# Kernel optimization log

Measured on AMD Instinct MI355X. Metric: run time of the kernel, lower is better.

## Reference

```python
import jax, jax.numpy as jnp
import numpy as np


def setup_inputs() -> dict:
    key = jax.random.key(0)
    k1, k2, k3, k4, k5 = jax.random.split(key, 5)
    B, K, S, E, I, D = 4, 2, 512, 8, 1024, 2048
    x = jax.random.normal(k1, (B, S, I), dtype=jnp.float32)
    weights = jax.random.uniform(k2, (B, K, S), dtype=jnp.float32)
    ensembles = jax.random.randint(k3, (B, K, S), 0, E, dtype=jnp.int64)
    # xavier_uniform-style init for expert weight tables
    lim1 = float(np.sqrt(6.0 / (D + I)))
    proj_in = jax.random.uniform(k4, (E, D, I), dtype=jnp.float32, minval=-lim1, maxval=lim1)
    proj_out = jax.random.uniform(k5, (E, I, D), dtype=jnp.float32, minval=-lim1, maxval=lim1)
    return {"x": x, "weights": weights, "ensembles": ensembles,
            "proj_in": proj_in, "proj_out": proj_out}


def reference(x, weights, ensembles, proj_in, proj_out):
    # x: (B,S,I); weights/ensembles: (B,K,S); proj_in: (E,D,I); proj_out: (E,I,D)
    # Same math as the torch module (dropout = identity in eval):
    #   per token t, out = sum_k w[k,t] * W2[e_kt] @ relu(W1[e_kt] @ x[t])
    # Computed as all-expert batched GEMMs + a gated (one-hot scatter) combine,
    # which is mathematically identical and avoids the (B,K,S,D,I) gather blowup.
    E = proj_in.shape[0]
    h = jax.nn.relu(jnp.einsum('edi,bsi->bsed', proj_in, x))      # (B,S,E,D)
    o = jnp.einsum('eid,bsed->bsei', proj_out, h)                 # (B,S,E,I)
    onehot = jax.nn.one_hot(ensembles, E, dtype=x.dtype)          # (B,K,S,E)
    gate = jnp.einsum('bks,bkse->bse', weights, onehot)           # (B,S,E)
    return jnp.einsum('bsei,bse->bsi', o, gate)                   # (B,S,I)
```

## Files before the change

kernel.cpp:

```cpp
#include <hip/hip_runtime.h>
#include <stdint.h>

#define THREADS 512
#define NE 8
#define BB 4
#define SS 512
#define KK 2
#define II 1024
#define DD 2048
#define NTOK (BB * SS)
#define NASSIGN (BB * KK * SS)

#define F4_X (NTOK * II / 4)
#define F4_P (NE * DD * II / 4)
#define CVB_X (F4_X / 1024)
#define CVB_P (F4_P / 1024)
#define CVB_TOTAL (CVB_X + 2 * CVB_P)

typedef unsigned short u16;
typedef __attribute__((ext_vector_type(8))) __bf16 bf16x8;
typedef __attribute__((ext_vector_type(4))) float f32x4;
typedef __attribute__((ext_vector_type(4))) unsigned int u32x4;

__device__ __forceinline__ u16 f32_to_bf16(float f) {
    unsigned int u = __builtin_bit_cast(unsigned int, f);
    unsigned int r = u + 0x7FFFu + ((u >> 16) & 1u);
    return (u16)(r >> 16);
}

__device__ __forceinline__ unsigned int pk2(float a, float b) {
    return (unsigned int)f32_to_bf16(a) | ((unsigned int)f32_to_bf16(b) << 16);
}

__device__ __forceinline__ void gload16(const void* g, void* l) {
    __builtin_amdgcn_global_load_lds(
        (const __attribute__((address_space(1))) unsigned int*)g,
        (__attribute__((address_space(3))) unsigned int*)l, 16, 0, 0);
}

#define BARRIER() do { \
    __builtin_amdgcn_sched_barrier(0); \
    __builtin_amdgcn_s_barrier(); \
    __builtin_amdgcn_sched_barrier(0); } while (0)

__device__ void setup_body(const void* __restrict__ ens_raw,
                           const float* __restrict__ weights,
                           int* __restrict__ meta,
                           int* __restrict__ tok,
                           float* __restrict__ wgt) {
    __shared__ int s_cnt[NE];
    __shared__ int s_cur[NE];
    __shared__ int s_flag;
    const int t = threadIdx.x;
    if (t < NE) s_cnt[t] = 0;
    if (t == 0) s_flag = 0;
    __syncthreads();

    const unsigned int* w32 = (const unsigned int*)ens_raw;
    unsigned int f = 0;
    for (int i = t; i < NASSIGN / 2; i += 256) f |= w32[2 * i + 1];
    if (f) atomicOr(&s_flag, 1);
    __syncthreads();
    const bool is32 = (s_flag != 0);
    const int* e32 = (const int*)ens_raw;
    const long long* e64 = (const long long*)ens_raw;

    for (int a = t; a < NASSIGN; a += 256) {
        int e = is32 ? e32[a] : (int)e64[a];
        atomicAdd(&s_cnt[e & 7], 1);
    }
    __syncthreads();

    if (t == 0) {
        int pb = 0, nt = 0;
        for (int e = 0; e < NE; e++) {
            int c = s_cnt[e];
            meta[8 + e] = c;
            meta[16 + e] = pb;
            s_cur[e] = pb;
            int n128 = (c + 127) >> 7;
            int pe = pb + n128 * 128;
            for (int i2 = 0; i2 < n128; i2 += 2) {
                meta[32 + nt] = e;
                meta[64 + nt] = pb + i2 * 128;
                meta[96 + nt] = pb + c;
                meta[128 + nt] = pe;
                nt++;
            }
            pb = pe;
        }
        meta[0] = nt;
        meta[1] = pb;
    }
    __syncthreads();

    for (int a = t; a < NASSIGN; a += 256) {
        int e = is32 ? e32[a] : (int)e64[a];
        e &= 7;
        int slot = atomicAdd(&s_cur[e], 1);
        int b = a >> 10;
        int s = a & (SS - 1);
        tok[slot] = b * SS + s;
        wgt[slot] = weights[a];
    }
    __syncthreads();

    for (int e = 0; e < NE; e++) {
        int st = meta[16 + e] + meta[8 + e];
        int en = (e < NE - 1) ? meta[16 + e + 1] : meta[1];
        for (int i = st + t; i < en; i += 256) {
            tok[i] = 0;
            wgt[i] = 0.f;
        }
    }
}

__global__ __launch_bounds__(256)
void convert_setup(const float* __restrict__ x,
                   const float* __restrict__ pin,
                   const float* __restrict__ pout,
                   u16* __restrict__ xb,
                   u16* __restrict__ pb1,
                   u16* __restrict__ pb2,
                   const void* __restrict__ ens,
                   const float* __restrict__ weights,
                   int* __restrict__ meta,
                   int* __restrict__ tok,
                   float* __restrict__ wgt) {
    const int b = blockIdx.x;
    if (b >= CVB_TOTAL) {
        setup_body(ens, weights, meta, tok, wgt);
        return;
    }
    const float* s;
    u16* d;
    size_t base;
    if (b < CVB_X)             { s = x;    d = xb;  base = (size_t)b * 1024; }
    else if (b < CVB_X + CVB_P){ s = pin;  d = pb1; base = (size_t)(b - CVB_X) * 1024; }
    else                       { s = pout; d = pb2; base = (size_t)(b - CVB_X - CVB_P) * 1024; }
    const f32x4* s4 = (const f32x4*)s;
    f32x4 v[4];
#pragma unroll
    for (int q = 0; q < 4; q++)
        v[q] = __builtin_nontemporal_load(&s4[base + q * 256 + threadIdx.x]);
#pragma unroll
    for (int q = 0; q < 4; q++) {
        uint2 o;
        o.x = pk2(v[q][0], v[q][1]);
        o.y = pk2(v[q][2], v[q][3]);
        *(uint2*)(d + 4 * (base + q * 256 + threadIdx.x)) = o;
    }
}

__global__ __launch_bounds__(THREADS, 2)
void gemm1(const u16* __restrict__ Abase,
           const u16* __restrict__ Bbase,
           const int* __restrict__ meta,
           const int* __restrict__ tok,
           u16* __restrict__ hdst) {
    constexpr int NT = II / 64;
    constexpr int ASZ = 256 * 64 * 2;
    constexpr int BUFSZ = 2 * ASZ;
    __shared__ char smem[2 * BUFSZ];

    const int lid = blockIdx.x;
    const int g = lid & 7;
    const int i = lid >> 3;
    const int tile = g + 8 * (i % 3);
    const int colt = i / 3;
    if (tile >= meta[0]) return;

    const int e     = meta[32 + tile];
    const int sbase = meta[64 + tile];
    const int wend  = meta[128 + tile];
    const int padmax = meta[1];
    const int colbase = colt * 256;

    const int tid = threadIdx.x;
    const int lane = tid & 63;
    const int wv = tid >> 6;
    const int wr = wv >> 2;
    const int wc = wv & 3;

    const u16* Bp = Bbase + (size_t)e * (size_t)(DD * II) + (size_t)colbase * II;

    int aoff[4], boff[4], cdst[4];
#pragma unroll
    for (int j = 0; j < 4; j++) {
        int c = j * 512 + tid;
        int row = c >> 3;
        int s = (c & 7) ^ (row & 7);
        cdst[j] = c * 16;
        int slot = sbase + row;
        if (slot > padmax - 1) slot = padmax - 1;
        aoff[j] = tok[slot] * II + s * 8;
        boff[j] = row * II + s * 8;
    }

    f32x4 acc[8][4];
#pragma unroll
    for (int m = 0; m < 8; m++)
#pragma unroll
        for (int n = 0; n < 4; n++)
            acc[m][n] = (f32x4){0.f, 0.f, 0.f, 0.f};

    auto STAGE = [&](int kt, char* buf) {
        const int kof = kt * 64;
#pragma unroll
        for (int j = 0; j < 4; j++)
            gload16(Abase + aoff[j] + kof, buf + cdst[j]);
#pragma unroll
        for (int j = 0; j < 4; j++)
            gload16(Bp + boff[j] + kof, buf + ASZ + cdst[j]);
    };

    auto COMPUTE = [&](const char* buf) {
        const u16* As = (const u16*)buf;
        const u16* Bs = (const u16*)(buf + ASZ);
#pragma unroll
        for (int kk = 0; kk < 2; kk++) {
            bf16x8 a[8], b[4];
#pragma unroll
            for (int m = 0; m < 8; m++) {
                int row = wr * 128 + m * 16 + (lane & 15);
                int slot = (kk * 4 + (lane >> 4)) ^ (row & 7);
                a[m] = *(const bf16x8*)&As[row * 64 + slot * 8];
            }
#pragma unroll
            for (int n = 0; n < 4; n++) {
                int col = wc * 64 + n * 16 + (lane & 15);
                int slot = (kk * 4 + (lane >> 4)) ^ (col & 7);
                b[n] = *(const bf16x8*)&Bs[col * 64 + slot * 8];
            }
            asm volatile("s_waitcnt lgkmcnt(0)" ::: "memory");
            __builtin_amdgcn_sched_barrier(0);
            __builtin_amdgcn_s_setprio(1);
#pragma unroll
            for (int m = 0; m < 8; m++)
#pragma unroll
                for (int n = 0; n < 4; n++)
                    acc[m][n] = __builtin_amdgcn_mfma_f32_16x16x32_bf16(
                        a[m], b[n], acc[m][n], 0, 0, 0);
            __builtin_amdgcn_s_setprio(0);
        }
    };

    char* buf0 = smem;
    char* buf1 = smem + BUFSZ;

    STAGE(0, buf0);
    asm volatile("s_waitcnt vmcnt(0)" ::: "memory");
    BARRIER();

#pragma unroll 1
    for (int t = 0; t < NT; ++t) {
        char* cur = (t & 1) ? buf1 : buf0;
        char* nxt = (t & 1) ? buf0 : buf1;
        const bool st = (t + 1 < NT);
        if (st) STAGE(t + 1, nxt);
        COMPUTE(cur);
        if (st) asm volatile("s_waitcnt vmcnt(0)" ::: "memory");
        BARRIER();
    }

#pragma unroll
    for (int m = 0; m < 8; m++) {
#pragma unroll
        for (int r = 0; r < 4; r++) {
            int row = wr * 128 + m * 16 + (lane >> 4) * 4 + r;
            int slot = sbase + row;
            if (slot < wend) {
                size_t ro = (size_t)slot * DD;
#pragma unroll
                for (int n = 0; n < 4; n++) {
                    int col = colbase + wc * 64 + n * 16 + (lane & 15);
                    float v = acc[m][n][r];
                    v = v > 0.f ? v : 0.f;
                    hdst[ro + col] = f32_to_bf16(v);
                }
            }
        }
    }
}

__global__ __launch_bounds__(THREADS, 2)
void gemm2(const u16* __restrict__ Abase,
           const u16* __restrict__ Bbase,
           const int* __restrict__ meta,
           const int* __restrict__ tok,
           const float* __restrict__ wgt,
           float* __restrict__ outdst) {
    constexpr int NT = DD / 64;
    constexpr int ASZ = 256 * 64 * 2;
    constexpr int BSZ = 128 * 64 * 2;
    constexpr int BUFSZ = ASZ + BSZ;
    __shared__ char smem[3 * BUFSZ];

    const int lid = blockIdx.x;
    const int g = lid & 7;
    const int i = lid >> 3;
    const int tile = g + 8 * (i % 3);
    const int colt = i / 3;
    if (tile >= meta[0]) return;

    const int e     = meta[32 + tile];
    const int sbase = meta[64 + tile];
    const int rend  = meta[96 + tile];
    const int padmax = meta[1];
    const int colbase = colt * 128;

    const int tid = threadIdx.x;
    const int lane = tid & 63;
    const int wv = tid >> 6;
    const int wr = wv >> 1;
    const int wc = wv & 1;

    const u16* Bp = Bbase + (size_t)e * (size_t)(DD * II) + (size_t)colbase * DD;

    int aoff[4], adst[4], boff[2], bdst[2];
#pragma unroll
    for (int j = 0; j < 4; j++) {
        int c = j * 512 + tid;
        int row = c >> 3;
        int s = (c & 7) ^ (row & 7);
        adst[j] = c * 16;
        int slot = sbase + row;
        if (slot > padmax - 1) slot = padmax - 1;
        aoff[j] = slot * DD + s * 8;
    }
#pragma unroll
    for (int j = 0; j < 2; j++) {
        int c = j * 512 + tid;
        int row = c >> 3;
        int s = (c & 7) ^ (row & 7);
        bdst[j] = c * 16;
        boff[j] = row * DD + s * 8;
    }

    f32x4 acc[4][4];
#pragma unroll
    for (int m = 0; m < 4; m++)
#pragma unroll
        for (int n = 0; n < 4; n++)
            acc[m][n] = (f32x4){0.f, 0.f, 0.f, 0.f};

    auto STAGE = [&](int kt, char* buf) {
        const int kof = kt * 64;
#pragma unroll
        for (int j = 0; j < 4; j++)
            gload16(Abase + aoff[j] + kof, buf + adst[j]);
#pragma unroll
        for (int j = 0; j < 2; j++)
            gload16(Bp + boff[j] + kof, buf + ASZ + bdst[j]);
    };

    auto COMPUTE = [&](const char* buf) {
        const u16* As = (const u16*)buf;
        const u16* Bs = (const u16*)(buf + ASZ);
        bf16x8 a[2][4], b[2][4];
#pragma unroll
        for (int kk = 0; kk < 2; kk++) {
#pragma unroll
            for (int m = 0; m < 4; m++) {
                int row = wr * 64 + m * 16 + (lane & 15);
                int slot = (kk * 4 + (lane >> 4)) ^ (row & 7);
                a[kk][m] = *(const bf16x8*)&As[row * 64 + slot * 8];
            }
#pragma unroll
            for (int n = 0; n < 4; n++) {
                int col = wc * 64 + n * 16 + (lane & 15);
                int slot = (kk * 4 + (lane >> 4)) ^ (col & 7);
                b[kk][n] = *(const bf16x8*)&Bs[col * 64 + slot * 8];
            }
        }
        asm volatile("s_waitcnt lgkmcnt(0)" ::: "memory");
        __builtin_amdgcn_sched_barrier(0);
        __builtin_amdgcn_s_setprio(1);
#pragma unroll
        for (int m = 0; m < 4; m++)
#pragma unroll
            for (int n = 0; n < 4; n++) {
                acc[m][n] = __builtin_amdgcn_mfma_f32_16x16x32_bf16(
                    a[0][m], b[0][n], acc[m][n], 0, 0, 0);
                acc[m][n] = __builtin_amdgcn_mfma_f32_16x16x32_bf16(
                    a[1][m], b[1][n], acc[m][n], 0, 0, 0);
            }
        __builtin_amdgcn_s_setprio(0);
    };

    char* pA = smem;
    char* pB = smem + BUFSZ;
    char* pC = smem + 2 * BUFSZ;

    STAGE(0, pA);
    STAGE(1, pB);
    asm volatile("s_waitcnt vmcnt(6)" ::: "memory");
    BARRIER();

#pragma unroll 1
    for (int t = 0; t < NT; ++t) {
        const bool st = (t + 2 < NT);
        if (st) STAGE(t + 2, pC);
        COMPUTE(pA);
        if (st) {
            asm volatile("s_waitcnt vmcnt(6)" ::: "memory");
        } else if (t + 1 < NT) {
            asm volatile("s_waitcnt vmcnt(0)" ::: "memory");
        }
        BARRIER();
        { char* tp = pA; pA = pB; pB = pC; pC = tp; }
    }

#pragma unroll
    for (int m = 0; m < 4; m++) {
#pragma unroll
        for (int r = 0; r < 4; r++) {
            int row = wr * 64 + m * 16 + (lane >> 4) * 4 + r;
            int slot = sbase + row;
            if (slot < rend) {
                float w = wgt[slot];
                size_t obase = (size_t)tok[slot] * II;
#pragma unroll
                for (int n = 0; n < 4; n++) {
                    int col = colbase + wc * 64 + n * 16 + (lane & 15);
                    atomicAdd(&outdst[obase + col], acc[m][n][r] * w);
                }
            }
        }
    }
}

extern "C" void kernel_launch(void* const* d_in, const int* in_sizes, int n_in,
                              void* d_out, int out_size, void* d_ws, size_t ws_size,
                              hipStream_t stream) {
    const float* x = (const float*)d_in[0];
    const float* weights = (const float*)d_in[1];
    const void* ens = d_in[2];
    const float* pin = (const float*)d_in[3];
    const float* pout = (const float*)d_in[4];
    float* out = (float*)d_out;

    char* ws = (char*)d_ws;
    int*   meta    = (int*)(ws);
    int*   tok     = (int*)(ws + 1024);
    float* wgt     = (float*)(ws + 21504);
    u16*   x_bf    = (u16*)(ws + 41984);
    u16*   pin_bf  = (u16*)(ws + 4236288);
    u16*   pout_bf = (u16*)(ws + 37790720);
    u16*   h       = (u16*)(ws + 71345152);

    hipMemsetAsync(d_out, 0, (size_t)out_size * sizeof(float), stream);

    convert_setup<<<dim3(CVB_TOTAL + 1), dim3(256), 0, stream>>>(
        x, pin, pout, x_bf, pin_bf, pout_bf, ens, weights, meta, tok, wgt);

    gemm1<<<dim3(8 * 3 * 8), dim3(THREADS), 0, stream>>>(
        x_bf, pin_bf, meta, tok, h);

    gemm2<<<dim3(8 * 3 * 8), dim3(THREADS), 0, stream>>>(
        h, pout_bf, meta, tok, wgt, out);
}
```

Before: 126.1 us.

## Overlap proj_out bf16 conversion with gemm1 via extra tail blocks

Moves the fp32-to-bf16 conversion of proj_out out of the setup kernel and into extra blocks appended to the gemm1 grid. Since gemm2 is the first consumer of the converted weights, that conversion can run concurrently with gemm1's compute blocks. This shortens the serial setup kernel, but the extra memory-bound blocks compete with gemm1 for bandwidth and CU slots.

New measurement: 120.8 us. 4.2% less time.

```diff
diff --git a/kernel.cpp b/kernel.cpp
--- a/kernel.cpp
+++ b/kernel.cpp
@@ -2,6 +2,7 @@
 #include <stdint.h>
 
 #define THREADS 512
+#define GRID1 (8 * 3 * 8)
 #define NE 8
 #define BB 4
 #define SS 512
@@ -15,7 +16,8 @@
 #define F4_P (NE * DD * II / 4)
 #define CVB_X (F4_X / 1024)
 #define CVB_P (F4_P / 1024)
-#define CVB_TOTAL (CVB_X + 2 * CVB_P)
+#define CVA_TOTAL (CVB_X + CVB_P)
+#define CVH_P (F4_P / 2048)
 
 typedef unsigned short u16;
 typedef __attribute__((ext_vector_type(8))) __bf16 bf16x8;
@@ -118,26 +120,23 @@
 __global__ __launch_bounds__(256)
 void convert_setup(const float* __restrict__ x,
                    const float* __restrict__ pin,
-                   const float* __restrict__ pout,
                    u16* __restrict__ xb,
                    u16* __restrict__ pb1,
-                   u16* __restrict__ pb2,
                    const void* __restrict__ ens,
                    const float* __restrict__ weights,
                    int* __restrict__ meta,
                    int* __restrict__ tok,
                    float* __restrict__ wgt) {
     const int b = blockIdx.x;
-    if (b >= CVB_TOTAL) {
+    if (b >= CVA_TOTAL) {
         setup_body(ens, weights, meta, tok, wgt);
         return;
     }
     const float* s;
     u16* d;
     size_t base;
-    if (b < CVB_X)             { s = x;    d = xb;  base = (size_t)b * 1024; }
-    else if (b < CVB_X + CVB_P){ s = pin;  d = pb1; base = (size_t)(b - CVB_X) * 1024; }
-    else                       { s = pout; d = pb2; base = (size_t)(b - CVB_X - CVB_P) * 1024; }
+    if (b < CVB_X) { s = x;   d = xb;  base = (size_t)b * 1024; }
+    else           { s = pin; d = pb1; base = (size_t)(b - CVB_X) * 1024; }
     const f32x4* s4 = (const f32x4*)s;
     f32x4 v[4];
 #pragma unroll
@@ -157,13 +156,32 @@
            const u16* __restrict__ Bbase,
            const int* __restrict__ meta,
            const int* __restrict__ tok,
-           u16* __restrict__ hdst) {
+           u16* __restrict__ hdst,
+           const float* __restrict__ pout,
+           u16* __restrict__ pout_bf) {
     constexpr int NT = II / 64;
     constexpr int ASZ = 256 * 64 * 2;
     constexpr int BUFSZ = 2 * ASZ;
     __shared__ char smem[2 * BUFSZ];
 
     const int lid = blockIdx.x;
+    if (lid >= GRID1) {
+        const size_t base = (size_t)(lid - GRID1) * 2048;
+        const f32x4* s4 = (const f32x4*)pout;
+        f32x4 v[4];
+#pragma unroll
+        for (int q = 0; q < 4; q++)
+            v[q] = __builtin_nontemporal_load(&s4[base + q * 512 + threadIdx.x]);
+#pragma unroll
+        for (int q = 0; q < 4; q++) {
+            uint2 o;
+            o.x = pk2(v[q][0], v[q][1]);
+            o.y = pk2(v[q][2], v[q][3]);
+            *(uint2*)(pout_bf + 4 * (base + q * 512 + threadIdx.x)) = o;
+        }
+        return;
+    }
+
     const int g = lid & 7;
     const int i = lid >> 3;
     const int tile = g + 8 * (i % 3);
@@ -451,11 +469,11 @@
 
     hipMemsetAsync(d_out, 0, (size_t)out_size * sizeof(float), stream);
 
-    convert_setup<<<dim3(CVB_TOTAL + 1), dim3(256), 0, stream>>>(
-        x, pin, pout, x_bf, pin_bf, pout_bf, ens, weights, meta, tok, wgt);
-
-    gemm1<<<dim3(8 * 3 * 8), dim3(THREADS), 0, stream>>>(
-        x_bf, pin_bf, meta, tok, h);
+    convert_setup<<<dim3(CVA_TOTAL + 1), dim3(256), 0, stream>>>(
+        x, pin, x_bf, pin_bf, ens, weights, meta, tok, wgt);
+
+    gemm1<<<dim3(GRID1 + CVH_P), dim3(THREADS), 0, stream>>>(
+        x_bf, pin_bf, meta, tok, h, pout, pout_bf);
 
     gemm2<<<dim3(8 * 3 * 8), dim3(THREADS), 0, stream>>>(
         h, pout_bf, meta, tok, wgt, out);
```
